# Kernel optimization log

Hardware: AMD Instinct MI355X
Metric: run time of the kernel (lower is better)

## Reference

```python
import jax, jax.numpy as jnp
import numpy as np

IN, H, T, B, HW = 2048, 512, 14, 256, 49

def setup_inputs() -> dict:
    key = jax.random.key(0)
    ks = jax.random.split(key, 10)
    s = 0.02
    return {
        "x": jax.random.normal(ks[0], (B, IN, HW), jnp.float32),
        "fixation": jax.random.randint(ks[1], (B, T), 0, HW, jnp.int64),
        # stacked gate weights, order: 0=input, 1=forget, 2=output, 3=memory
        "Wx": jax.random.normal(ks[2], (4, H, IN), jnp.float32) * s,
        "bx": jnp.zeros((4, H), jnp.float32),
        "Wh": jax.random.normal(ks[3], (4, H, H), jnp.float32) * s,
        "bh": jnp.zeros((4, H), jnp.float32),
        # peephole weights, order: 0=input_c, 1=forget_c, 2=output_c
        "Wc": jax.random.normal(ks[4], (3, H, H), jnp.float32) * s,
        "bc": jnp.zeros((3, H), jnp.float32),
        "Wd": jax.random.normal(ks[5], (1, H), jnp.float32) * s,
        "bd": jnp.zeros((1,), jnp.float32),
    }

def reference(x, fixation, Wx, bx, Wh, bh, Wc, bc, Wd, bd):
    batch, feat, hw = x.shape
    seq_len = fixation.shape[1]
    # process_lengths: padding token is index 0
    lengths = seq_len - jnp.sum(fixation == 0, axis=1)  # [B]
    # gather fixated feature columns: [B, feat, T] -> [B, T, feat]
    xg = jnp.take_along_axis(x, fixation[:, None, :], axis=2)
    xg = jnp.transpose(xg, (0, 2, 1))
    # precompute all input projections for all 4 gates: [B, T, 4, H]
    xproj = jnp.einsum('btf,ghf->btgh', xg, Wx) + bx

    def step(carry, xp):  # xp: [B, 4, H]
        h, c = carry
        hp = jnp.einsum('bk,ghk->bgh', h, Wh) + bh  # [B, 4, H]
        i = jax.nn.sigmoid(xp[:, 0] + hp[:, 0] + c @ Wc[0].T + bc[0])
        f = jax.nn.sigmoid(xp[:, 1] + hp[:, 1] + c @ Wc[1].T + bc[1])
        g = jnp.tanh(xp[:, 3] + hp[:, 3])
        next_c = f * c + i * g
        o = jax.nn.sigmoid(xp[:, 2] + hp[:, 2] + next_c @ Wc[2].T + bc[2])
        h = o * next_c
        return (h, next_c), h

    hidden = Wx.shape[1]
    init = (jnp.zeros((batch, hidden), x.dtype), jnp.zeros((batch, hidden), x.dtype))
    _, hs = jax.lax.scan(step, init, jnp.transpose(xproj, (1, 0, 2, 3)))  # [T, B, H]
    hs = jnp.transpose(hs, (1, 0, 2))  # [B, T, H]
    # crop_seq: select hidden at end of each valid sequence
    last = hs[jnp.arange(batch), lengths - 1]  # [B, H]
    return jax.nn.sigmoid(last @ Wd.T + bd)  # [B, 1]
```

## Files before the change

kernel.cpp:

```cpp
#include <hip/hip_runtime.h>
#include <cstdint>
#include <cstddef>

#define B_   256
#define T_   14
#define INF_ 2048
#define H_   512
#define HW_  49
#define NG_  2048
#define KC_  1024
#define NBLK 256

typedef __attribute__((ext_vector_type(8))) _Float16 f16x8;
typedef __attribute__((ext_vector_type(4))) float f32x4;
typedef _Float16 f16;

typedef const void __attribute__((address_space(1))) gvoid_t;
typedef void __attribute__((address_space(3))) svoid_t;

__device__ __forceinline__ void async16(const void* g, void* l) {
  __builtin_amdgcn_global_load_lds((gvoid_t*)g, (svoid_t*)l, 16, 0, 0);
}

__device__ __forceinline__ float sigm(float x) { return 1.0f / (1.0f + __expf(-x)); }

__device__ __forceinline__ float aload(const float* p) {
  return __hip_atomic_load(p, __ATOMIC_RELAXED, __HIP_MEMORY_SCOPE_AGENT);
}
__device__ __forceinline__ unsigned long long aload64(const void* p) {
  return __hip_atomic_load((const unsigned long long*)p, __ATOMIC_RELAXED, __HIP_MEMORY_SCOPE_AGENT);
}
__device__ __forceinline__ void astore(float* p, float v) {
  __hip_atomic_store(p, v, __ATOMIC_RELAXED, __HIP_MEMORY_SCOPE_AGENT);
}
__device__ __forceinline__ void astore32(void* p, unsigned v) {
  __hip_atomic_store((unsigned*)p, v, __ATOMIC_RELAXED, __HIP_MEMORY_SCOPE_AGENT);
}

__device__ __forceinline__ void gbarG(int* __restrict__ gb, const int p) {
  __syncthreads();
  if (threadIdx.x == 0) {
    asm volatile("s_waitcnt vmcnt(0)" ::: "memory");
    if (__hip_atomic_fetch_add(gb, 1, __ATOMIC_RELAXED, __HIP_MEMORY_SCOPE_AGENT) == (p << 5) + 31) {
      __hip_atomic_store(gb + 16, p + 1, __ATOMIC_RELAXED, __HIP_MEMORY_SCOPE_AGENT);
    } else {
      while (__hip_atomic_load(gb + 16, __ATOMIC_RELAXED, __HIP_MEMORY_SCOPE_AGENT) <= p)
        __builtin_amdgcn_s_sleep(1);
    }
  }
  __syncthreads();
}

__global__ void k_prep(const float* __restrict__ Wx, const float* __restrict__ bx,
                       const float* __restrict__ Wh, const float* __restrict__ Wc,
                       const float* __restrict__ bh, const float* __restrict__ bc,
                       const int* __restrict__ fix,
                       f16* __restrict__ Wxh, float* __restrict__ bxp,
                       f16* __restrict__ Wbig, f16* __restrict__ Wc2h,
                       float* __restrict__ biasb, int* __restrict__ flag64)
{
  __shared__ int any;
  const int tid = blockIdx.x * blockDim.x + threadIdx.x;
  const int nth = gridDim.x * blockDim.x;
  if (blockIdx.x == 0) {
    if (threadIdx.x == 0) any = 0;
    __syncthreads();
    int a = 0;
    for (int j = 1 + 2 * (int)threadIdx.x; j < B_ * T_; j += 2 * (int)blockDim.x) a |= fix[j];
    if (a) any = 1;
    __syncthreads();
    if (threadIdx.x == 0) flag64[0] = (any == 0) ? 1 : 0;
  }
  for (int i = tid; i < 4 * H_ * INF_; i += nth) {
    const int n = i >> 11, k = i & 2047;
    const int g = n & 3, h = n >> 2;
    Wxh[i] = (f16)Wx[((size_t)(g * H_ + h)) * INF_ + k];
  }
  for (int i = tid; i < NG_ * KC_; i += nth) {
    const int n = i >> 10, k = i & 1023;
    const int g = n & 3, h = n >> 2;
    float v;
    if (k < H_) v = Wh[((size_t)(g * H_ + h)) * H_ + k];
    else {
      const int kk = k - H_;
      v = (g == 0) ? Wc[h * H_ + kk] : (g == 1) ? Wc[H_ * H_ + h * H_ + kk] : 0.0f;
    }
    Wbig[i] = (f16)v;
  }
  for (int i = tid; i < H_ * H_; i += nth) Wc2h[i] = (f16)Wc[2 * H_ * H_ + i];
  for (int i = tid; i < NG_; i += nth) {
    const int g = i & 3, h = i >> 2;
    biasb[i] = bh[g * H_ + h] + ((g == 0) ? bc[h] : (g == 1) ? bc[H_ + h] : 0.0f);
    bxp[i] = bx[g * H_ + h];
  }
}

__global__ __launch_bounds__(256) void k_gather(const float* __restrict__ x,
                                                const int* __restrict__ fix,
                                                const int* __restrict__ flag64,
                                                f16* __restrict__ xg,
                                                int* __restrict__ tlast)
{
  __shared__ float rows[256 * 49];
  __shared__ int wv[T_];
  const int b = blockIdx.x;
  const int tid = threadIdx.x;
  const int is64 = flag64[0];
  if (tid < T_) wv[tid] = is64 ? fix[2 * (b * T_ + tid)] : fix[b * T_ + tid];
  __syncthreads();
  if (blockIdx.y == 0 && tid == 0) {
    int cnt = 0;
    for (int t = 0; t < T_; ++t) cnt += (wv[t] == 0);
    tlast[b] = (cnt < T_) ? (T_ - 1 - cnt) : (T_ - 1);
  }
  const float* xb = x + (size_t)b * (INF_ * HW_);
  for (int c = 0; c < 2; ++c) {
    const int ch = blockIdx.y * 2 + c;
    if (c) __syncthreads();
    const float4* src = (const float4*)(xb + (size_t)ch * 256 * 49);
    float4* dst4 = (float4*)rows;
    for (int i = tid; i < 3136; i += 256) dst4[i] = src[i];
    __syncthreads();
#pragma unroll
    for (int t = 0; t < T_; ++t)
      xg[(size_t)(b * T_ + t) * INF_ + ch * 256 + tid] = (f16)rows[tid * 49 + wv[t]];
  }
}

__global__ __launch_bounds__(256) void k_gemm_big(
    const f16* __restrict__ A, const f16* __restrict__ Bw,
    const float* __restrict__ bxp, float* __restrict__ Cproj)
{
  __shared__ alignas(16) f16 As[128 * 64];
  __shared__ alignas(16) f16 Bs[128 * 64];
  const int tid = threadIdx.x;
  const int lane = tid & 63;
  const int w = tid >> 6;
  const int wm = w >> 1, wn = w & 1;
  const int flat = blockIdx.y * 16 + blockIdx.x;
  const int wg = (flat & 7) * 56 + (flat >> 3);
  const int m0 = (wg >> 4) * 128, n0 = (wg & 15) * 128;
  f32x4 acc[4][4] = {};
  const int lrow = lane >> 3;
  const int kg = lane & 7;
  for (int ks = 0; ks < 2048; ks += 64) {
#pragma unroll
    for (int q = 0; q < 4; ++q) {
      const int chunk = (w << 2) + q;
      const int row = (chunk << 3) + lrow;
      const int skg = kg ^ (row & 7);
      async16(A + (size_t)(m0 + row) * 2048 + ks + (skg << 3), As + chunk * 512);
      async16(Bw + (size_t)(n0 + row) * 2048 + ks + (skg << 3), Bs + chunk * 512);
    }
    __syncthreads();
#pragma unroll
    for (int kk = 0; kk < 2; ++kk) {
      const int kgl = (kk << 2) + (lane >> 4);
      f16x8 af[4], bf[4];
#pragma unroll
      for (int mi = 0; mi < 4; ++mi) {
        const int r = (wm << 6) + (mi << 4) + (lane & 15);
        af[mi] = *(const f16x8*)(As + r * 64 + ((kgl ^ (r & 7)) << 3));
      }
#pragma unroll
      for (int ni = 0; ni < 4; ++ni) {
        const int r = (wn << 6) + (ni << 4) + (lane & 15);
        bf[ni] = *(const f16x8*)(Bs + r * 64 + ((kgl ^ (r & 7)) << 3));
      }
#pragma unroll
      for (int mi = 0; mi < 4; ++mi)
#pragma unroll
        for (int ni = 0; ni < 4; ++ni)
          acc[mi][ni] = __builtin_amdgcn_mfma_f32_16x16x32_f16(af[mi], bf[ni], acc[mi][ni], 0, 0, 0);
    }
    __syncthreads();
  }
#pragma unroll
  for (int mi = 0; mi < 4; ++mi)
#pragma unroll
    for (int ni = 0; ni < 4; ++ni)
#pragma unroll
      for (int r4 = 0; r4 < 4; ++r4) {
        const int row = m0 + (wm << 6) + (mi << 4) + ((lane >> 4) << 2) + r4;
        const int col = n0 + (wn << 6) + (ni << 4) + (lane & 15);
        Cproj[(size_t)row * 2048 + col] = acc[mi][ni][r4] + bxp[col];
      }
}

__global__ __launch_bounds__(256, 1) void k_recur(
    const f16* __restrict__ Wbig, const f16* __restrict__ Wc2h,
    const float* __restrict__ biasb, const float* __restrict__ bc,
    const float* __restrict__ xproj, f16* __restrict__ h16,
    f16* __restrict__ cb16, float* __restrict__ lasth,
    const int* __restrict__ tlast, const float* __restrict__ Wd,
    const float* __restrict__ bd, float* __restrict__ out,
    int* __restrict__ bar)
{
  __shared__ alignas(16) f16 hT[32 * 512];
  __shared__ alignas(16) f16 cT[32 * 512];
  __shared__ alignas(16) float exch[1024];
  __shared__ alignas(16) float ex2[1024];
  const int tid = threadIdx.x, lane = tid & 63, w = tid >> 6;
  const int wm = w >> 1, wn = w & 1;
  const int lk = lane >> 4;
  const int bid = blockIdx.x;
  const int grp = bid >> 5, grank = bid & 31;
  const int m0 = grp * 32;
  const int n0A = grank * 64;
  const int n0h = grank * 16;
  int* const gb = bar + grp * 64;

  f16x8 wG[2][32];
#pragma unroll
  for (int ni = 0; ni < 2; ++ni) {
    const f16* src = Wbig + (size_t)(n0A + wn * 32 + ni * 16 + (lane & 15)) * 1024 + (lk << 3);
#pragma unroll
    for (int kc = 0; kc < 32; ++kc) wG[ni][kc] = *(const f16x8*)(src + kc * 32);
  }
  f16x8 wO[8];
  {
    const f16* src = Wc2h + (size_t)(n0h + (lane & 15)) * 512 + (lk << 3);
#pragma unroll
    for (int j = 0; j < 8; ++j) wO[j] = *(const f16x8*)(src + (wn * 8 + j) * 32);
  }
  const int hq = (lane >> 2) & 3;
  const int browA = wm * 16 + (lk << 2) + (lane & 3);
  const int bgA = m0 + browA;
  float4 b4c[2];
#pragma unroll
  for (int ni = 0; ni < 2; ++ni)
    b4c[ni] = *(const float4*)(biasb + 4 * (n0h + wn * 8 + ni * 4 + hq));
  const int colg = n0h + (lane & 15);
  const float bco = bc[1024 + colg];
  int tl2[4] = {-1, -1, -1, -1};
  if (w < 2) {
#pragma unroll
    for (int r4 = 0; r4 < 4; ++r4) tl2[r4] = tlast[m0 + w * 16 + lk * 4 + r4];
  }
  {
    const f16x8 z = {};
#pragma unroll
    for (int j = 0; j < 8; ++j) *(f16x8*)(cT + (((j << 8) + tid) << 3)) = z;
  }
  float creg[2] = {0.f, 0.f};
  __syncthreads();

  for (int t = 0; t < T_; ++t) {
    float4 x4p[2];
#pragma unroll
    for (int ni = 0; ni < 2; ++ni)
      x4p[ni] = *(const float4*)(xproj + (size_t)(bgA * T_ + t) * 2048 +
                                 4 * (n0h + wn * 8 + ni * 4 + hq));
#pragma unroll
    for (int j = 0; j < 8; ++j) {
      const int u = (j << 8) + tid;
      const int row = u >> 6, kg = u & 63;
      const f16* src = h16 + (size_t)(m0 + row) * 512 + (kg << 3);
      union { f16x8 v; unsigned long long q[2]; } u2;
      u2.q[0] = aload64(src);
      u2.q[1] = aload64(src + 4);
      *(f16x8*)(hT + row * 512 + ((kg >> 3) << 6) + (((kg & 7) ^ (row & 7)) << 3)) = u2.v;
    }
    __syncthreads();
    f32x4 acc[4][2] = {};
    {
      const int ra = wm * 16 + (lane & 15);
#pragma unroll
      for (int kc = 0; kc < 32; ++kc) {
        const int kgl = ((kc & 1) << 2) + lk;
        const f16* base = (kc < 16) ? (hT + ((kc >> 1) << 6)) : (cT + (((kc - 16) >> 1) << 6));
        const f16x8 af = *(const f16x8*)(base + ra * 512 + ((kgl ^ (ra & 7)) << 3));
        acc[kc & 3][0] = __builtin_amdgcn_mfma_f32_16x16x32_f16(af, wG[0][kc], acc[kc & 3][0], 0, 0, 0);
        acc[kc & 3][1] = __builtin_amdgcn_mfma_f32_16x16x32_f16(af, wG[1][kc], acc[kc & 3][1], 0, 0, 0);
      }
    }
    __syncthreads();
#pragma unroll
    for (int ni = 0; ni < 2; ++ni) {
      const f32x4 a = (acc[0][ni] + acc[1][ni]) + (acc[2][ni] + acc[3][ni]);
      float a0 = a[0], a1 = a[1], a2 = a[2], a3 = a[3];
      {
        const bool odd = lane & 1;
        float xx = odd ? a0 : a1, yy = odd ? a2 : a3;
        xx = __shfl_xor(xx, 1); yy = __shfl_xor(yy, 1);
        if (odd) { a0 = xx; a2 = yy; } else { a1 = xx; a3 = yy; }
      }
      {
        const bool hi = lane & 2;
        float xx = hi ? a0 : a2, yy = hi ? a1 : a3;
        xx = __shfl_xor(xx, 2); yy = __shfl_xor(yy, 2);
        if (hi) { a0 = xx; a1 = yy; } else { a2 = xx; a3 = yy; }
      }
      const int hl = wn * 8 + ni * 4 + hq;
      const float gi = a0 + b4c[ni].x + x4p[ni].x;
      const float gf = a1 + b4c[ni].y + x4p[ni].y;
      const float go = a2 + b4c[ni].z + x4p[ni].z;
      const float gm = a3 + b4c[ni].w + x4p[ni].w;
      const float cn = sigm(gi) * tanhf(gm) + sigm(gf) * creg[ni];
      creg[ni] = cn;
      exch[browA * 16 + hl] = cn;
      exch[512 + browA * 16 + hl] = go;
    }
    __syncthreads();
    {
      const int rowe = tid >> 3, pr = tid & 7;
      const float2 cp = *(const float2*)(exch + rowe * 16 + (pr << 1));
      union { unsigned u; f16 h2[2]; } pk;
      pk.h2[0] = (f16)cp.x; pk.h2[1] = (f16)cp.y;
      astore32(cb16 + (size_t)(m0 + rowe) * 512 + n0h + (pr << 1), pk.u);
    }
    gbarG(gb, 2 * t);

#pragma unroll
    for (int j = 0; j < 8; ++j) {
      const int u = (j << 8) + tid;
      const int row = u >> 6, kg = u & 63;
      const f16* src = cb16 + (size_t)(m0 + row) * 512 + (kg << 3);
      union { f16x8 v; unsigned long long q[2]; } u2;
      u2.q[0] = aload64(src);
      u2.q[1] = aload64(src + 4);
      *(f16x8*)(cT + row * 512 + ((kg >> 3) << 6) + (((kg & 7) ^ (row & 7)) << 3)) = u2.v;
    }
    __syncthreads();
    f32x4 accB[2] = {};
    {
      const int ra2 = wm * 16 + (lane & 15);
#pragma unroll
      for (int j = 0; j < 8; ++j) {
        const int kc = wn * 8 + j;
        const int kgl = ((kc & 1) << 2) + lk;
        const f16x8 af = *(const f16x8*)(cT + ra2 * 512 + ((kc >> 1) << 6) + ((kgl ^ (ra2 & 7)) << 3));
        accB[j & 1] = __builtin_amdgcn_mfma_f32_16x16x32_f16(af, wO[j], accB[j & 1], 0, 0, 0);
      }
    }
    {
      const f32x4 s2 = accB[0] + accB[1];
#pragma unroll
      for (int r4 = 0; r4 < 4; ++r4)
        ex2[w * 256 + (lk * 4 + r4) * 16 + (lane & 15)] = s2[r4];
    }
    __syncthreads();
    if (w < 2) {
#pragma unroll
      for (int r4 = 0; r4 < 4; ++r4) {
        const int brow = w * 16 + lk * 4 + r4;
        const int idx = (lk * 4 + r4) * 16 + (lane & 15);
        const float sum = ex2[(2 * w) * 256 + idx] + ex2[(2 * w + 1) * 256 + idx];
        const float go = exch[512 + brow * 16 + (lane & 15)];
        const float cn = (float)cT[brow * 512 + ((colg >> 6) << 6) +
                                   ((((colg >> 3) & 7) ^ (brow & 7)) << 3) + (colg & 7)];
        const float hv = sigm(sum + go + bco) * cn;
        const float hvo = __shfl_xor(hv, 1);
        if (!(lane & 1)) {
          union { unsigned u; f16 h2[2]; } pk;
          pk.h2[0] = (f16)hv; pk.h2[1] = (f16)hvo;
          astore32(h16 + (size_t)(m0 + brow) * 512 + (colg & ~1), pk.u);
        }
        if (t == tl2[r4]) astore(lasth + (size_t)(m0 + brow) * 512 + colg, hv);
      }
    }
    gbarG(gb, 2 * t + 1);
  }

  if (w == 0) {
    const int b = m0 + grank;
    float s = 0.f;
#pragma unroll
    for (int k = lane; k < 512; k += 64) s += aload(lasth + (size_t)b * 512 + k) * Wd[k];
#pragma unroll
    for (int off = 32; off > 0; off >>= 1) s += __shfl_down(s, off);
    if (lane == 0) out[b] = 1.0f / (1.0f + __expf(-(s + bd[0])));
  }
}

extern "C" void kernel_launch(void* const* d_in, const int* in_sizes, int n_in,
                              void* d_out, int out_size, void* d_ws, size_t ws_size,
                              hipStream_t stream) {
  const float* x   = (const float*)d_in[0];
  const int*   fix = (const int*)d_in[1];
  const float* Wx  = (const float*)d_in[2];
  const float* bx  = (const float*)d_in[3];
  const float* Wh  = (const float*)d_in[4];
  const float* bh  = (const float*)d_in[5];
  const float* Wc  = (const float*)d_in[6];
  const float* bc  = (const float*)d_in[7];
  const float* Wd  = (const float*)d_in[8];
  const float* bd  = (const float*)d_in[9];
  float* out = (float*)d_out;
  char* ws = (char*)d_ws;

  f16*   xg    = (f16*)(ws);
  f16*   Wxh   = (f16*)(ws + 14680064);
  float* xproj = (float*)(ws + 23068672);
  f16*   Wbig  = (f16*)(ws + 52428800);
  f16*   Wc2h  = (f16*)(ws + 56623104);
  float* biasb = (float*)(ws + 57147392);
  float* bxp   = (float*)(ws + 57155584);
  f16*   h16   = (f16*)(ws + 57163776);
  f16*   cb16  = (f16*)(ws + 57425920);
  float* lasth = (float*)(ws + 57688064);
  int*   tlast = (int*)(ws + 58212352);
  int*   flag64= (int*)(ws + 58213376);
  int*   bar   = (int*)(ws + 58213440);

  hipMemsetAsync(h16, 0, 262144, stream);
  hipMemsetAsync(cb16, 0, 262144, stream);
  hipMemsetAsync(bar, 0, 4096, stream);

  k_prep<<<2048, 256, 0, stream>>>(Wx, bx, Wh, Wc, bh, bc, fix, Wxh, bxp, Wbig, Wc2h, biasb, flag64);
  k_gather<<<dim3(256, 4), 256, 0, stream>>>(x, fix, flag64, xg, tlast);
  k_gemm_big<<<dim3(16, 28), 256, 0, stream>>>(xg, Wxh, bxp, xproj);
  k_recur<<<NBLK, 256, 0, stream>>>(Wbig, Wc2h, biasb, bc, xproj, h16, cb16,
                                    lasth, tlast, Wd, bd, out, bar);
}
```

Measured before the change: 235.3 us.

## Split recurrence into two independent 16-row sub-tiles with per-block slot flags

Each block now handles its 32 batch rows as two independent 16-row tiles that advance in turns, so work on one tile can overlap another block's progress on the other. The counter-based group barrier is replaced by per-block progress slots that each wavefront polls with a warp vote. Waves are re-split so each one covers 16 gate columns across the full K range, which halves the weight registers each wave holds. The cost is more __syncthreads per step, and correctness now depends on the relaxed-atomic slot protocol and on the initial state of the slot array.

```diff
diff --git a/kernel.cpp b/kernel.cpp
--- a/kernel.cpp
+++ b/kernel.cpp
@@ -37,18 +37,13 @@
   __hip_atomic_store((unsigned*)p, v, __ATOMIC_RELAXED, __HIP_MEMORY_SCOPE_AGENT);
 }
 
-__device__ __forceinline__ void gbarG(int* __restrict__ gb, const int p) {
-  __syncthreads();
-  if (threadIdx.x == 0) {
-    asm volatile("s_waitcnt vmcnt(0)" ::: "memory");
-    if (__hip_atomic_fetch_add(gb, 1, __ATOMIC_RELAXED, __HIP_MEMORY_SCOPE_AGENT) == (p << 5) + 31) {
-      __hip_atomic_store(gb + 16, p + 1, __ATOMIC_RELAXED, __HIP_MEMORY_SCOPE_AGENT);
-    } else {
-      while (__hip_atomic_load(gb + 16, __ATOMIC_RELAXED, __HIP_MEMORY_SCOPE_AGENT) <= p)
-        __builtin_amdgcn_s_sleep(1);
-    }
-  }
-  __syncthreads();
+__device__ __forceinline__ void waitSlots(const int* slots, const int target) {
+  const int* p = slots + (threadIdx.x & 31);
+  for (;;) {
+    const int v = __hip_atomic_load(p, __ATOMIC_RELAXED, __HIP_MEMORY_SCOPE_AGENT);
+    if (__all(v >= target)) break;
+    __builtin_amdgcn_s_sleep(1);
+  }
 }
 
 __global__ void k_prep(const float* __restrict__ Wx, const float* __restrict__ bx,
@@ -196,51 +191,42 @@
     const float* __restrict__ bd, float* __restrict__ out,
     int* __restrict__ bar)
 {
-  __shared__ alignas(16) f16 hT[32 * 512];
-  __shared__ alignas(16) f16 cT[32 * 512];
-  __shared__ alignas(16) float exch[1024];
-  __shared__ alignas(16) float ex2[1024];
+  __shared__ alignas(16) f16 hT[2][16 * 512];
+  __shared__ alignas(16) f16 cT[2][16 * 512];
+  __shared__ alignas(16) float exCN[256];
+  __shared__ alignas(16) float exGO[2][256];
+  __shared__ alignas(16) float ex2[4 * 256];
   const int tid = threadIdx.x, lane = tid & 63, w = tid >> 6;
-  const int wm = w >> 1, wn = w & 1;
   const int lk = lane >> 4;
   const int bid = blockIdx.x;
-  const int grp = bid >> 5, grank = bid & 31;
-  const int m0 = grp * 32;
-  const int n0A = grank * 64;
-  const int n0h = grank * 16;
-  int* const gb = bar + grp * 64;
-
-  f16x8 wG[2][32];
-#pragma unroll
-  for (int ni = 0; ni < 2; ++ni) {
-    const f16* src = Wbig + (size_t)(n0A + wn * 32 + ni * 16 + (lane & 15)) * 1024 + (lk << 3);
-#pragma unroll
-    for (int kc = 0; kc < 32; ++kc) wG[ni][kc] = *(const f16x8*)(src + kc * 32);
-  }
-  f16x8 wO[8];
+  const int pair = bid >> 5, grank = bid & 31;
+  const int n0A = grank * 64, n0h = grank * 16;
+  const int m0t[2] = {pair * 32, pair * 32 + 16};
+  int* const sl[2] = {bar + (2 * pair) * 64, bar + (2 * pair + 1) * 64};
+
+  f16x8 wG[32];
+  {
+    const f16* src = Wbig + (size_t)(n0A + w * 16 + (lane & 15)) * 1024 + (lk << 3);
+#pragma unroll
+    for (int kc = 0; kc < 32; ++kc) wG[kc] = *(const f16x8*)(src + kc * 32);
+  }
+  f16x8 wO[4];
   {
     const f16* src = Wc2h + (size_t)(n0h + (lane & 15)) * 512 + (lk << 3);
 #pragma unroll
-    for (int j = 0; j < 8; ++j) wO[j] = *(const f16x8*)(src + (wn * 8 + j) * 32);
+    for (int j = 0; j < 4; ++j) wO[j] = *(const f16x8*)(src + (w * 4 + j) * 32);
   }
   const int hq = (lane >> 2) & 3;
-  const int browA = wm * 16 + (lk << 2) + (lane & 3);
-  const int bgA = m0 + browA;
-  float4 b4c[2];
-#pragma unroll
-  for (int ni = 0; ni < 2; ++ni)
-    b4c[ni] = *(const float4*)(biasb + 4 * (n0h + wn * 8 + ni * 4 + hq));
-  const int colg = n0h + (lane & 15);
-  const float bco = bc[1024 + colg];
-  int tl2[4] = {-1, -1, -1, -1};
-  if (w < 2) {
-#pragma unroll
-    for (int r4 = 0; r4 < 4; ++r4) tl2[r4] = tlast[m0 + w * 16 + lk * 4 + r4];
-  }
+  const int browA = (lk << 2) + (lane & 3);
+  const int hlA = w * 4 + hq;
+  const float4 b4c = *(const float4*)(biasb + 4 * (n0h + hlA));
+  const int rowB = tid >> 4, colB = tid & 15;
+  const float bco = bc[1024 + n0h + colB];
+  const int tlB[2] = {tlast[m0t[0] + rowB], tlast[m0t[1] + rowB]};
   {
     const f16x8 z = {};
 #pragma unroll
-    for (int j = 0; j < 8; ++j) *(f16x8*)(cT + (((j << 8) + tid) << 3)) = z;
+    for (int j = 0; j < 8; ++j) *(f16x8*)(&cT[0][0] + (((j << 8) + tid) << 3)) = z;
   }
   float creg[2] = {0.f, 0.f};
   __syncthreads();
@@ -248,122 +234,128 @@
   for (int t = 0; t < T_; ++t) {
     float4 x4p[2];
 #pragma unroll
-    for (int ni = 0; ni < 2; ++ni)
-      x4p[ni] = *(const float4*)(xproj + (size_t)(bgA * T_ + t) * 2048 +
-                                 4 * (n0h + wn * 8 + ni * 4 + hq));
-#pragma unroll
-    for (int j = 0; j < 8; ++j) {
-      const int u = (j << 8) + tid;
-      const int row = u >> 6, kg = u & 63;
-      const f16* src = h16 + (size_t)(m0 + row) * 512 + (kg << 3);
-      union { f16x8 v; unsigned long long q[2]; } u2;
-      u2.q[0] = aload64(src);
-      u2.q[1] = aload64(src + 4);
-      *(f16x8*)(hT + row * 512 + ((kg >> 3) << 6) + (((kg & 7) ^ (row & 7)) << 3)) = u2.v;
+    for (int tt = 0; tt < 2; ++tt)
+      x4p[tt] = *(const float4*)(xproj + (size_t)((m0t[tt] + browA) * T_ + t) * 2048 +
+                                 4 * (n0h + hlA));
+
+#pragma unroll
+    for (int tt = 0; tt < 2; ++tt) {
+      if (t) waitSlots(sl[tt], 2 * t);
+#pragma unroll
+      for (int j = 0; j < 4; ++j) {
+        const int u = (j << 8) + tid;
+        const int row = u >> 6, kg = u & 63;
+        const f16* src = h16 + (size_t)(m0t[tt] + row) * 512 + (kg << 3);
+        union { f16x8 v; unsigned long long q[2]; } u2;
+        u2.q[0] = aload64(src);
+        u2.q[1] = aload64(src + 4);
+        *(f16x8*)(&hT[tt][0] + row * 512 + ((kg >> 3) << 6) + (((kg & 7) ^ (row & 7)) << 3)) = u2.v;
+      }
+      __syncthreads();
+      f32x4 acc[2] = {};
+      {
+        const int ra = lane & 15;
+#pragma unroll
+        for (int kc = 0; kc < 32; ++kc) {
+          const int kgl = ((kc & 1) << 2) + lk;
+          const f16* base = (kc < 16) ? (&hT[tt][0] + ((kc >> 1) << 6))
+                                      : (&cT[tt][0] + (((kc - 16) >> 1) << 6));
+          const f16x8 af = *(const f16x8*)(base + ra * 512 + ((kgl ^ (ra & 7)) << 3));
+          acc[kc & 1] = __builtin_amdgcn_mfma_f32_16x16x32_f16(af, wG[kc], acc[kc & 1], 0, 0, 0);
+        }
+      }
+      {
+        const f32x4 a = acc[0] + acc[1];
+        float a0 = a[0], a1 = a[1], a2 = a[2], a3 = a[3];
+        {
+          const bool odd = lane & 1;
+          float xx = odd ? a0 : a1, yy = odd ? a2 : a3;
+          xx = __shfl_xor(xx, 1); yy = __shfl_xor(yy, 1);
+          if (odd) { a0 = xx; a2 = yy; } else { a1 = xx; a3 = yy; }
+        }
+        {
+          const bool hi = lane & 2;
+          float xx = hi ? a0 : a2, yy = hi ? a1 : a3;
+          xx = __shfl_xor(xx, 2); yy = __shfl_xor(yy, 2);
+          if (hi) { a0 = xx; a1 = yy; } else { a2 = xx; a3 = yy; }
+        }
+        const float gi = a0 + b4c.x + x4p[tt].x;
+        const float gf = a1 + b4c.y + x4p[tt].y;
+        const float go = a2 + b4c.z + x4p[tt].z;
+        const float gm = a3 + b4c.w + x4p[tt].w;
+        const float cn = sigm(gi) * tanhf(gm) + sigm(gf) * creg[tt];
+        creg[tt] = cn;
+        exCN[browA * 16 + hlA] = cn;
+        exGO[tt][browA * 16 + hlA] = go;
+      }
+      __syncthreads();
+      if (tid < 128) {
+        const int rowe = tid >> 3, pr = tid & 7;
+        const float2 cp = *(const float2*)(exCN + rowe * 16 + (pr << 1));
+        union { unsigned u; f16 h2[2]; } pk;
+        pk.h2[0] = (f16)cp.x; pk.h2[1] = (f16)cp.y;
+        astore32(cb16 + (size_t)(m0t[tt] + rowe) * 512 + n0h + (pr << 1), pk.u);
+      }
+      __syncthreads();
+      if (tid == 0)
+        __hip_atomic_store(sl[tt] + grank, 2 * t + 1, __ATOMIC_RELAXED, __HIP_MEMORY_SCOPE_AGENT);
     }
-    __syncthreads();
-    f32x4 acc[4][2] = {};
-    {
-      const int ra = wm * 16 + (lane & 15);
-#pragma unroll
-      for (int kc = 0; kc < 32; ++kc) {
-        const int kgl = ((kc & 1) << 2) + lk;
-        const f16* base = (kc < 16) ? (hT + ((kc >> 1) << 6)) : (cT + (((kc - 16) >> 1) << 6));
-        const f16x8 af = *(const f16x8*)(base + ra * 512 + ((kgl ^ (ra & 7)) << 3));
-        acc[kc & 3][0] = __builtin_amdgcn_mfma_f32_16x16x32_f16(af, wG[0][kc], acc[kc & 3][0], 0, 0, 0);
-        acc[kc & 3][1] = __builtin_amdgcn_mfma_f32_16x16x32_f16(af, wG[1][kc], acc[kc & 3][1], 0, 0, 0);
-      }
-    }
-    __syncthreads();
-#pragma unroll
-    for (int ni = 0; ni < 2; ++ni) {
-      const f32x4 a = (acc[0][ni] + acc[1][ni]) + (acc[2][ni] + acc[3][ni]);
-      float a0 = a[0], a1 = a[1], a2 = a[2], a3 = a[3];
+
+#pragma unroll
+    for (int tt = 0; tt < 2; ++tt) {
+      waitSlots(sl[tt], 2 * t + 1);
+#pragma unroll
+      for (int j = 0; j < 4; ++j) {
+        const int u = (j << 8) + tid;
+        const int row = u >> 6, kg = u & 63;
+        const f16* src = cb16 + (size_t)(m0t[tt] + row) * 512 + (kg << 3);
+        union { f16x8 v; unsigned long long q[2]; } u2;
+        u2.q[0] = aload64(src);
+        u2.q[1] = aload64(src + 4);
+        *(f16x8*)(&cT[tt][0] + row * 512 + ((kg >> 3) << 6) + (((kg & 7) ^ (row & 7)) << 3)) = u2.v;
+      }
+      __syncthreads();
+      f32x4 accB = {};
       {
-        const bool odd = lane & 1;
-        float xx = odd ? a0 : a1, yy = odd ? a2 : a3;
-        xx = __shfl_xor(xx, 1); yy = __shfl_xor(yy, 1);
-        if (odd) { a0 = xx; a2 = yy; } else { a1 = xx; a3 = yy; }
-      }
+        const int ra = lane & 15;
+#pragma unroll
+        for (int j = 0; j < 4; ++j) {
+          const int kc = w * 4 + j;
+          const int kgl = ((kc & 1) << 2) + lk;
+          const f16x8 af = *(const f16x8*)(&cT[tt][0] + ra * 512 + ((kc >> 1) << 6) +
+                                           ((kgl ^ (ra & 7)) << 3));
+          accB = __builtin_amdgcn_mfma_f32_16x16x32_f16(af, wO[j], accB, 0, 0, 0);
+        }
+      }
+#pragma unroll
+      for (int r4 = 0; r4 < 4; ++r4)
+        ex2[w * 256 + ((lk << 2) + r4) * 16 + (lane & 15)] = accB[r4];
+      __syncthreads();
       {
-        const bool hi = lane & 2;
-        float xx = hi ? a0 : a2, yy = hi ? a1 : a3;
-        xx = __shfl_xor(xx, 2); yy = __shfl_xor(yy, 2);
-        if (hi) { a0 = xx; a1 = yy; } else { a2 = xx; a3 = yy; }
-      }
-      const int hl = wn * 8 + ni * 4 + hq;
-      const float gi = a0 + b4c[ni].x + x4p[ni].x;
-      const float gf = a1 + b4c[ni].y + x4p[ni].y;
-      const float go = a2 + b4c[ni].z + x4p[ni].z;
-      const float gm = a3 + b4c[ni].w + x4p[ni].w;
-      const float cn = sigm(gi) * tanhf(gm) + sigm(gf) * creg[ni];
-      creg[ni] = cn;
-      exch[browA * 16 + hl] = cn;
-      exch[512 + browA * 16 + hl] = go;
-    }
-    __syncthreads();
-    {
-      const int rowe = tid >> 3, pr = tid & 7;
-      const float2 cp = *(const float2*)(exch + rowe * 16 + (pr << 1));
-      union { unsigned u; f16 h2[2]; } pk;
-      pk.h2[0] = (f16)cp.x; pk.h2[1] = (f16)cp.y;
-      astore32(cb16 + (size_t)(m0 + rowe) * 512 + n0h + (pr << 1), pk.u);
-    }
-    gbarG(gb, 2 * t);
-
-#pragma unroll
-    for (int j = 0; j < 8; ++j) {
-      const int u = (j << 8) + tid;
-      const int row = u >> 6, kg = u & 63;
-      const f16* src = cb16 + (size_t)(m0 + row) * 512 + (kg << 3);
-      union { f16x8 v; unsigned long long q[2]; } u2;
-      u2.q[0] = aload64(src);
-      u2.q[1] = aload64(src + 4);
-      *(f16x8*)(cT + row * 512 + ((kg >> 3) << 6) + (((kg & 7) ^ (row & 7)) << 3)) = u2.v;
-    }
-    __syncthreads();
-    f32x4 accB[2] = {};
-    {
-      const int ra2 = wm * 16 + (lane & 15);
-#pragma unroll
-      for (int j = 0; j < 8; ++j) {
-        const int kc = wn * 8 + j;
-        const int kgl = ((kc & 1) << 2) + lk;
-        const f16x8 af = *(const f16x8*)(cT + ra2 * 512 + ((kc >> 1) << 6) + ((kgl ^ (ra2 & 7)) << 3));
-        accB[j & 1] = __builtin_amdgcn_mfma_f32_16x16x32_f16(af, wO[j], accB[j & 1], 0, 0, 0);
-      }
-    }
-    {
-      const f32x4 s2 = accB[0] + accB[1];
-#pragma unroll
-      for (int r4 = 0; r4 < 4; ++r4)
-        ex2[w * 256 + (lk * 4 + r4) * 16 + (lane & 15)] = s2[r4];
-    }
-    __syncthreads();
-    if (w < 2) {
-#pragma unroll
-      for (int r4 = 0; r4 < 4; ++r4) {
-        const int brow = w * 16 + lk * 4 + r4;
-        const int idx = (lk * 4 + r4) * 16 + (lane & 15);
-        const float sum = ex2[(2 * w) * 256 + idx] + ex2[(2 * w + 1) * 256 + idx];
-        const float go = exch[512 + brow * 16 + (lane & 15)];
-        const float cn = (float)cT[brow * 512 + ((colg >> 6) << 6) +
-                                   ((((colg >> 3) & 7) ^ (brow & 7)) << 3) + (colg & 7)];
-        const float hv = sigm(sum + go + bco) * cn;
+        const int ib = rowB * 16 + colB;
+        const float sum = (ex2[ib] + ex2[256 + ib]) + (ex2[512 + ib] + ex2[768 + ib]);
+        const int cg = n0h + colB;
+        const float cn = (float)cT[tt][rowB * 512 + ((cg >> 6) << 6) +
+                                       ((((cg >> 3) & 7) ^ (rowB & 7)) << 3) + (cg & 7)];
+        const float hv = sigm(sum + exGO[tt][ib] + bco) * cn;
         const float hvo = __shfl_xor(hv, 1);
-        if (!(lane & 1)) {
+        if (!(tid & 1)) {
           union { unsigned u; f16 h2[2]; } pk;
           pk.h2[0] = (f16)hv; pk.h2[1] = (f16)hvo;
-          astore32(h16 + (size_t)(m0 + brow) * 512 + (colg & ~1), pk.u);
+          astore32(h16 + (size_t)(m0t[tt] + rowB) * 512 + (cg & ~1), pk.u);
         }
-        if (t == tl2[r4]) astore(lasth + (size_t)(m0 + brow) * 512 + colg, hv);
-      }
+        if (t == tlB[tt]) astore(lasth + (size_t)(m0t[tt] + rowB) * 512 + cg, hv);
+      }
+      __syncthreads();
+      if (tid == 0)
+        __hip_atomic_store(sl[tt] + grank, 2 * t + 2, __ATOMIC_RELAXED, __HIP_MEMORY_SCOPE_AGENT);
     }
-    gbarG(gb, 2 * t + 1);
-  }
-
+  }
+
+  waitSlots(sl[0], 2 * T_);
+  waitSlots(sl[1], 2 * T_);
   if (w == 0) {
-    const int b = m0 + grank;
+    const int b = pair * 32 + grank;
     float s = 0.f;
 #pragma unroll
     for (int k = lane; k < 512; k += 64) s += aload(lasth + (size_t)b * 512 + k) * Wd[k];
```

Result: faster. 217.9 us (-7.4%).
